# Performance work log

Measured on AMD Instinct MI355X. Metric: run time of the kernel, lower is better.

## Reference

```python
import jax, jax.numpy as jnp
import numpy as np

EPS = 1e-5
LOCAL_WINDOW = 256
NUM_HEADS = 16


def _layernorm(x, g, b):
    m = jnp.mean(x, axis=-1, keepdims=True)
    v = jnp.mean(jnp.square(x - m), axis=-1, keepdims=True)
    return (x - m) * jax.lax.rsqrt(v + EPS) * g + b


def _rotate_half(x):
    x1, x2 = jnp.split(x, 2, axis=-1)
    return jnp.concatenate([-x2, x1], axis=-1)


def _rope_cos_sin(s, d, base=10000.0):
    half = d // 2
    inv_freq = 1.0 / base ** (jnp.arange(half, dtype=jnp.float32) / float(half))
    t = jnp.arange(s, dtype=jnp.float32)
    freqs = jnp.einsum('s,d->sd', t, inv_freq)          # [s, half]
    emb = jnp.concatenate([freqs, freqs], axis=-1)       # [s, d]
    return jnp.cos(emb)[None, None, :, :], jnp.sin(emb)[None, None, :, :]


def setup_inputs() -> dict:
    key = jax.random.key(0)
    ks = jax.random.split(key, 8)
    B, S, D, F = 2, 2048, 1024, 4096
    sc = lambda d: 1.0 / np.sqrt(d)
    return {
        'x': jax.random.normal(ks[0], (B, S, D), jnp.float32),
        'w_qkv': jax.random.normal(ks[1], (D, 3 * D), jnp.float32) * sc(D),
        'w_out': jax.random.normal(ks[2], (D, D), jnp.float32) * sc(D),
        'g1': jnp.ones((D,), jnp.float32),
        'b1': jnp.zeros((D,), jnp.float32),
        'g2': jnp.ones((D,), jnp.float32),
        'b2': jnp.zeros((D,), jnp.float32),
        'w_gate': jax.random.normal(ks[3], (D, F), jnp.float32) * sc(D),
        'b_gate': jnp.zeros((F,), jnp.float32),
        'w_up': jax.random.normal(ks[4], (D, F), jnp.float32) * sc(D),
        'b_up': jnp.zeros((F,), jnp.float32),
        'w_down': jax.random.normal(ks[5], (F, D), jnp.float32) * sc(F),
        'b_down': jnp.zeros((D,), jnp.float32),
    }


def reference(x, w_qkv, w_out, g1, b1, g2, b2, w_gate, b_gate, w_up, b_up, w_down, b_down):
    B, S, D = x.shape
    H = NUM_HEADS
    hd = D // H

    # ---- pre-norm + RoPE self-attention ----
    y = _layernorm(x, g1, b1)
    qkv = jnp.einsum('bsd,de->bse', y, w_qkv)
    q, k, v = jnp.split(qkv, 3, axis=-1)
    split_heads = lambda t: t.reshape(B, S, H, hd).transpose(0, 2, 1, 3)  # [b,h,s,hd]
    q, k, v = split_heads(q), split_heads(k), split_heads(v)

    cos, sin = _rope_cos_sin(S, hd)
    q = q * cos + _rotate_half(q) * sin
    k = k * cos + _rotate_half(k) * sin

    scale = float(hd) ** -0.5
    logits = jnp.einsum('bhid,bhjd->bhij', q, k) * scale

    i = jnp.arange(S)[:, None]
    j = jnp.arange(S)[None, :]
    can = (jnp.abs(j - i) <= LOCAL_WINDOW) & (j <= i)    # local + causal band
    logits = jnp.where(can[None, None], logits, jnp.float32(-1e9))

    attn = jax.nn.softmax(logits, axis=-1)
    o = jnp.einsum('bhij,bhjd->bhid', attn, v)
    o = o.transpose(0, 2, 1, 3).reshape(B, S, D)
    x = x + jnp.einsum('bsd,de->bse', o, w_out)

    # ---- pre-norm + SwiGLU MLP ----
    y = _layernorm(x, g2, b2)
    gate = jnp.einsum('bsd,df->bsf', y, w_gate) + b_gate
    up = jnp.einsum('bsd,df->bsf', y, w_up) + b_up
    gated = gate * jax.nn.silu(up)
    x = x + jnp.einsum('bsf,fd->bsd', gated, w_down) + b_down
    return x
```

## Files before the change

### kernel.cpp

```cpp
#include <hip/hip_runtime.h>

typedef unsigned short u16;
typedef unsigned long long u64;
typedef __attribute__((ext_vector_type(8))) short bf16x8;
typedef __attribute__((ext_vector_type(4))) float f32x4;

__device__ inline u16 f2bf(float f) {
  unsigned int u = __float_as_uint(f);
  u += 0x7fffu + ((u >> 16) & 1u);
  return (u16)(u >> 16);
}
__device__ inline float bf2f(u16 h) { return __uint_as_float(((unsigned int)h) << 16); }

__device__ inline void gload_lds16(const void* gp, void* lp) {
  __builtin_amdgcn_global_load_lds(
      (const __attribute__((address_space(1))) unsigned int*)gp,
      (__attribute__((address_space(3))) unsigned int*)lp, 16, 0, 0);
}

__global__ __launch_bounds__(256) void ln_kernel(const float* __restrict__ x,
                                                 const float* __restrict__ g,
                                                 const float* __restrict__ beta,
                                                 u16* __restrict__ y) {
  __shared__ float red[8];
  const int row = blockIdx.x;
  const int t = threadIdx.x;
  const float4 xv = *(const float4*)(x + (long)row * 1024 + t * 4);
  float s = xv.x + xv.y + xv.z + xv.w;
  float sq = xv.x * xv.x + xv.y * xv.y + xv.z * xv.z + xv.w * xv.w;
#pragma unroll
  for (int d = 1; d < 64; d <<= 1) {
    s += __shfl_xor(s, d);
    sq += __shfl_xor(sq, d);
  }
  if ((t & 63) == 0) { red[t >> 6] = s; red[4 + (t >> 6)] = sq; }
  __syncthreads();
  s = red[0] + red[1] + red[2] + red[3];
  sq = red[4] + red[5] + red[6] + red[7];
  const float mean = s * (1.f / 1024.f);
  const float var = sq * (1.f / 1024.f) - mean * mean;
  const float inv = rsqrtf(var + 1e-5f);
  float xe[4] = {xv.x, xv.y, xv.z, xv.w};
  u16 ov[4];
#pragma unroll
  for (int e = 0; e < 4; ++e)
    ov[e] = f2bf((xe[e] - mean) * inv * g[t * 4 + e] + beta[t * 4 + e]);
  *(u64*)(y + (long)row * 1024 + t * 4) = *(u64*)ov;
}

__global__ __launch_bounds__(256) void transpose_bf16(const float* __restrict__ in,
                                                      u16* __restrict__ out,
                                                      int R, int C) {
  __shared__ float tile[64][33];
  const int t = threadIdx.x;
  const int tx = t & 31, ty = t >> 5;
  const int rx = t & 63, cy = t >> 6;
  const long r0 = (long)blockIdx.y * 64, c0 = (long)blockIdx.x * 32;
#pragma unroll
  for (int i = 0; i < 8; ++i)
    tile[ty + i * 8][tx] = in[(r0 + ty + i * 8) * C + c0 + tx];
  __syncthreads();
#pragma unroll
  for (int i = 0; i < 8; ++i)
    out[(c0 + i * 4 + cy) * R + r0 + rx] = f2bf(tile[rx][i * 4 + cy]);
}

__global__ __launch_bounds__(256) void transpose_v(const u16* __restrict__ vv,
                                                   u16* __restrict__ vt) {
  __shared__ u16 tile[64][72];
  const int bh = blockIdx.y;
  const long s0 = (long)blockIdx.x * 64;
  const int t = threadIdx.x;
  const int r = t >> 3, cc = (t & 7) * 8;
  const long src = ((long)(bh >> 4) * 2048 + s0) * 1024 + (bh & 15) * 64;
  *(bf16x8*)&tile[r][cc] = *(const bf16x8*)(vv + src + (long)r * 1024 + cc);
  *(bf16x8*)&tile[r + 32][cc] = *(const bf16x8*)(vv + src + (long)(r + 32) * 1024 + cc);
  __syncthreads();
  const int d = t >> 3, sx = (t & 7) * 8;
  u16 o0[8], o1[8];
#pragma unroll
  for (int e = 0; e < 8; ++e) { o0[e] = tile[sx + e][d]; o1[e] = tile[sx + e][d + 32]; }
  const long dst = (long)bh * 64 * 2048 + s0;
  *(bf16x8*)(vt + dst + (long)d * 2048 + sx) = *(bf16x8*)o0;
  *(bf16x8*)(vt + dst + (long)(d + 32) * 2048 + sx) = *(bf16x8*)o1;
}

__global__ __launch_bounds__(256) void rope_kernel(const u16* __restrict__ qkv,
                                                   u16* __restrict__ qr,
                                                   u16* __restrict__ kr,
                                                   u16* __restrict__ vv) {
  const int row = blockIdx.x;
  const int s = row & 2047;
  const int t = threadIdx.x;
  const u16* base = qkv + (long)row * 3072;
  const long orow = (long)row * 1024;
#pragma unroll
  for (int rep = 0; rep < 2; ++rep) {
    const int p = rep * 256 + t;
    const int h = p >> 5, d0 = p & 31;
    const float inv = exp2f((float)d0 * (-13.287712379549449f / 32.f));
    const float ang = (float)s * inv;
    float sn, cs;
    sincosf(ang, &sn, &cs);
    const int c1 = h * 64 + d0, c2 = c1 + 32;
    float x1 = bf2f(base[c1]), x2 = bf2f(base[c2]);
    qr[orow + c1] = f2bf((x1 * cs - x2 * sn) * 0.125f);
    qr[orow + c2] = f2bf((x2 * cs + x1 * sn) * 0.125f);
    float y1 = bf2f(base[1024 + c1]), y2 = bf2f(base[1024 + c2]);
    kr[orow + c1] = f2bf(y1 * cs - y2 * sn);
    kr[orow + c2] = f2bf(y2 * cs + y1 * sn);
  }
  *(u64*)(vv + orow + t * 4) = *(const u64*)(base + 2048 + t * 4);
}

__global__ __launch_bounds__(64, 4) void attn_kernel(const u16* __restrict__ qr,
                                                     const u16* __restrict__ kr,
                                                     const u16* __restrict__ vt,
                                                     u16* __restrict__ o) {
  __shared__ __attribute__((aligned(16))) u16 Pl[16][40];
  int wg = blockIdx.x;
  wg = (wg & 7) * 512 + (wg >> 3);
  const int qt = wg & 127;
  const int bh = wg >> 7;
  const int qs = qt * 16;
  const int l = threadIdx.x;
  const int lr = l & 15, lg = l >> 4;
  const long bho = (long)(bh >> 4) * 2048 * 1024 + (long)(bh & 15) * 64;
  const long vtb = (long)bh * 64 * 2048;

  const u16* qp = qr + bho + (long)(qs + lr) * 1024 + lg * 8;
  const bf16x8 aq0 = *(const bf16x8*)qp;
  const bf16x8 aq1 = *(const bf16x8*)(qp + 32);

  f32x4 oacc[4];
#pragma unroll
  for (int nt = 0; nt < 4; ++nt) { oacc[nt][0] = 0.f; oacc[nt][1] = 0.f; oacc[nt][2] = 0.f; oacc[nt][3] = 0.f; }
  float m_[4], ls[4];
#pragma unroll
  for (int r = 0; r < 4; ++r) { m_[r] = -1e30f; ls[r] = 0.f; }

  for (int ch = 0; ch < 9; ++ch) {
    const int j0 = qs - 256 + ch * 32;
    if (j0 + 32 <= 0) continue;

    const int jc0u = j0 + lr;
    const int jc1u = j0 + 16 + lr;
    const int jc0 = min(max(jc0u, 0), 2047);
    const int jc1 = min(max(jc1u, 0), 2047);
    const u16* kp0 = kr + bho + (long)jc0 * 1024 + lg * 8;
    const u16* kp1 = kr + bho + (long)jc1 * 1024 + lg * 8;
    const bf16x8 b00 = *(const bf16x8*)kp0;
    const bf16x8 b01 = *(const bf16x8*)(kp0 + 32);
    const bf16x8 b10 = *(const bf16x8*)kp1;
    const bf16x8 b11 = *(const bf16x8*)(kp1 + 32);

    f32x4 z; z[0] = 0.f; z[1] = 0.f; z[2] = 0.f; z[3] = 0.f;
    f32x4 s0 = __builtin_amdgcn_mfma_f32_16x16x32_bf16(aq0, b00, z, 0, 0, 0);
    s0 = __builtin_amdgcn_mfma_f32_16x16x32_bf16(aq1, b01, s0, 0, 0, 0);
    f32x4 s1 = __builtin_amdgcn_mfma_f32_16x16x32_bf16(aq0, b10, z, 0, 0, 0);
    s1 = __builtin_amdgcn_mfma_f32_16x16x32_bf16(aq1, b11, s1, 0, 0, 0);

    float p0[4], p1[4], al[4];
#pragma unroll
    for (int r = 0; r < 4; ++r) {
      const int qg = qs + lg * 4 + r;
      const bool v0 = (jc0u >= 0) & (jc0u <= qg) & (qg - jc0u <= 256);
      const bool v1 = (jc1u >= 0) & (jc1u <= qg) & (qg - jc1u <= 256);
      const float t0 = v0 ? s0[r] : -1e30f;
      const float t1 = v1 ? s1[r] : -1e30f;
      float mx = fmaxf(t0, t1);
      mx = fmaxf(mx, __shfl_xor(mx, 1));
      mx = fmaxf(mx, __shfl_xor(mx, 2));
      mx = fmaxf(mx, __shfl_xor(mx, 4));
      mx = fmaxf(mx, __shfl_xor(mx, 8));
      const float mn = fmaxf(m_[r], mx);
      if (mn < -1e29f) {
        al[r] = 1.f; p0[r] = 0.f; p1[r] = 0.f;
      } else {
        al[r] = __expf(m_[r] - mn);
        p0[r] = (t0 < -1e29f) ? 0.f : __expf(t0 - mn);
        p1[r] = (t1 < -1e29f) ? 0.f : __expf(t1 - mn);
      }
      m_[r] = mn;
      float rs = p0[r] + p1[r];
      rs += __shfl_xor(rs, 1);
      rs += __shfl_xor(rs, 2);
      rs += __shfl_xor(rs, 4);
      rs += __shfl_xor(rs, 8);
      ls[r] = ls[r] * al[r] + rs;
    }
#pragma unroll
    for (int r = 0; r < 4; ++r) {
      Pl[lg * 4 + r][lr] = f2bf(p0[r]);
      Pl[lg * 4 + r][lr + 16] = f2bf(p1[r]);
    }
    asm volatile("s_waitcnt lgkmcnt(0)" ::: "memory");
    const bf16x8 pa = *(const bf16x8*)(&Pl[lr][lg * 8]);

    const int jb = min(max(j0 + lg * 8, 0), 2040);
    const u16* vp = vt + vtb + (long)lr * 2048 + jb;
#pragma unroll
    for (int nt = 0; nt < 4; ++nt) {
      const bf16x8 bv = *(const bf16x8*)(vp + (long)(nt * 16) * 2048);
      f32x4 oa = oacc[nt];
#pragma unroll
      for (int r = 0; r < 4; ++r) oa[r] *= al[r];
      oacc[nt] = __builtin_amdgcn_mfma_f32_16x16x32_bf16(pa, bv, oa, 0, 0, 0);
    }
  }
#pragma unroll
  for (int nt = 0; nt < 4; ++nt)
#pragma unroll
    for (int r = 0; r < 4; ++r) {
      const long qg = qs + lg * 4 + r;
      o[bho + qg * 1024 + nt * 16 + lr] = f2bf(oacc[nt][r] / ls[r]);
    }
}

__device__ __forceinline__ void stage_half(u16* lds, int ldsbase,
                                           const u16* gp, int ld, int col,
                                           int tid, int w) {
  const int r0 = tid >> 3;
  const int sw = ((tid & 7) ^ (r0 & 7)) << 3;
  gload_lds16(gp + (long)r0 * ld + col + sw, lds + ldsbase + w * 512);
  gload_lds16(gp + (long)(r0 + 64) * ld + col + sw, lds + ldsbase + 4096 + w * 512);
}

template <int EPI>
__global__ __launch_bounds__(512, 2) void gemm8p(const u16* __restrict__ A,
                                                 const u16* __restrict__ BT,
                                                 u16* __restrict__ Cb,
                                                 const float* __restrict__ bias,
                                                 const u16* __restrict__ gate,
                                                 float* __restrict__ Cf0,
                                                 float* __restrict__ Cf1,
                                                 int M, int N, int Kfull, int Kl) {
  __shared__ __attribute__((aligned(16))) u16 lds[65536];
  const int tid = threadIdx.x;
  const int w = tid >> 6, l = tid & 63;
  const int lr = l & 15, lg = l >> 4;
  const int l7 = l & 7;
  const int wr = w >> 2, wc = w & 3;
  const int nbx = N >> 8, nby = M >> 8;
  int wg = blockIdx.x;
  { const int cpx = gridDim.x >> 3; wg = (wg & 7) * cpx + (wg >> 3); }
  const int z = wg / (nbx * nby);
  const int rem = wg % (nbx * nby);
  const long m0 = (long)(rem / nbx) * 256;
  const long n0 = (long)(rem % nbx) * 256;
  const long koff = (long)z * Kl;
  const int NT = Kl >> 6;

  f32x4 acc[8][4];
#pragma unroll
  for (int i = 0; i < 8; ++i)
#pragma unroll
    for (int j = 0; j < 4; ++j) { acc[i][j][0] = 0.f; acc[i][j][1] = 0.f; acc[i][j][2] = 0.f; acc[i][j][3] = 0.f; }

  const u16* Alo = A + m0 * Kfull + koff;
  const u16* Ahi = A + (m0 + 128) * Kfull + koff;
  const u16* Blo = BT + n0 * Kfull + koff;
  const u16* Bhi = BT + (n0 + 128) * Kfull + koff;

  stage_half(lds, 0, Alo, Kfull, 0, tid, w);
  stage_half(lds, 8192, Ahi, Kfull, 0, tid, w);
  stage_half(lds, 32768, Blo, Kfull, 0, tid, w);
  stage_half(lds, 40960, Bhi, Kfull, 0, tid, w);
  stage_half(lds, 49152, Blo, Kfull, 64, tid, w);
  stage_half(lds, 57344, Bhi, Kfull, 64, tid, w);
  asm volatile("s_waitcnt vmcnt(4)" ::: "memory");
  __builtin_amdgcn_s_barrier();

  for (int t = 0; t < NT; ++t) {
    const int p = t & 1;
    const int baA = (p * 2 + wr) * 8192;
    const int bB = 32768 + p * 16384;
    bf16x8 b[4][2];
#pragma unroll
    for (int q = 0; q < 4; ++q) {
      bf16x8 a[2][2];
#pragma unroll
      for (int m2 = 0; m2 < 2; ++m2) {
        const int rowA = (q * 2 + m2) * 16 + lr;
#pragma unroll
        for (int kh = 0; kh < 2; ++kh)
          a[m2][kh] = *(const bf16x8*)(lds + baA + rowA * 64 + (((kh * 4 + lg) ^ l7) << 3));
      }
      if (q == 0) {
#pragma unroll
        for (int fn = 0; fn < 4; ++fn) {
          const int rb = wc * 64 + fn * 16 + lr;
#pragma unroll
          for (int kh = 0; kh < 2; ++kh)
            b[fn][kh] = *(const bf16x8*)(lds + bB + (rb >> 7) * 8192 + (rb & 127) * 64 + (((kh * 4 + lg) ^ l7) << 3));
        }
      }
      if (q == 0 && t + 1 < NT) stage_half(lds, ((p ^ 1) * 2 + 0) * 8192, Alo, Kfull, (t + 1) * 64, tid, w);
      if (q == 1 && t + 1 < NT) stage_half(lds, ((p ^ 1) * 2 + 1) * 8192, Ahi, Kfull, (t + 1) * 64, tid, w);
      if (q == 2 && t + 2 < NT) stage_half(lds, 32768 + (p * 2 + 0) * 8192, Blo, Kfull, (t + 2) * 64, tid, w);
      if (q == 3 && t + 2 < NT) stage_half(lds, 32768 + (p * 2 + 1) * 8192, Bhi, Kfull, (t + 2) * 64, tid, w);

      __builtin_amdgcn_s_barrier();
      asm volatile("s_waitcnt lgkmcnt(0)" ::: "memory");
      __builtin_amdgcn_s_setprio(1);
#pragma unroll
      for (int m2 = 0; m2 < 2; ++m2)
#pragma unroll
        for (int fn = 0; fn < 4; ++fn)
#pragma unroll
          for (int kh = 0; kh < 2; ++kh)
            acc[q * 2 + m2][fn] = __builtin_amdgcn_mfma_f32_16x16x32_bf16(a[m2][kh], b[fn][kh], acc[q * 2 + m2][fn], 0, 0, 0);
      __builtin_amdgcn_s_setprio(0);
      if (q == 3) {
        if (t + 2 < NT) { asm volatile("s_waitcnt vmcnt(4)" ::: "memory"); }
        else            { asm volatile("s_waitcnt vmcnt(0)" ::: "memory"); }
      }
      __builtin_amdgcn_s_barrier();
    }
  }

  float* Cf = nullptr;
  if constexpr (EPI == 0) Cf = (z < 2 ? Cf0 : Cf1) + (long)(z & 1) * M * N;

#pragma unroll
  for (int fm = 0; fm < 8; ++fm) {
    const long mr = m0 + wr * 128 + fm * 16 + lg * 4;
#pragma unroll
    for (int fn = 0; fn < 4; ++fn) {
      const long nc = n0 + wc * 64 + fn * 16 + lr;
#pragma unroll
      for (int r = 0; r < 4; ++r) {
        const long idx = (mr + r) * N + nc;
        const float v = acc[fm][fn][r];
        if constexpr (EPI == 5) {
          Cb[idx] = f2bf(v);
        } else if constexpr (EPI == 2) {
          Cb[idx] = f2bf(v + bias[nc]);
        } else if constexpr (EPI == 3) {
          const float u = v + bias[nc];
          const float sg = 1.f / (1.f + __expf(-u));
          Cb[idx] = f2bf(bf2f(gate[idx]) * u * sg);
        } else {
          Cf[idx] = v;
        }
      }
    }
  }
}

__global__ __launch_bounds__(256) void combine_ln(const float* __restrict__ p0,
                                                  const float* __restrict__ p1,
                                                  const float* __restrict__ x,
                                                  const float* __restrict__ g,
                                                  const float* __restrict__ beta,
                                                  float* __restrict__ x1,
                                                  u16* __restrict__ y) {
  __shared__ float red[8];
  const long MN = (long)4096 * 1024;
  const int row = blockIdx.x;
  const int t = threadIdx.x;
  const long base = (long)row * 1024 + t * 4;
  const float4 a = *(const float4*)(p0 + base);
  const float4 b = *(const float4*)(p0 + MN + base);
  const float4 c = *(const float4*)(p1 + base);
  const float4 d = *(const float4*)(p1 + MN + base);
  const float4 r = *(const float4*)(x + base);
  float v[4] = {a.x + b.x + c.x + d.x + r.x, a.y + b.y + c.y + d.y + r.y,
                a.z + b.z + c.z + d.z + r.z, a.w + b.w + c.w + d.w + r.w};
  *(float4*)(x1 + base) = *(float4*)v;
  float s = v[0] + v[1] + v[2] + v[3];
  float sq = v[0] * v[0] + v[1] * v[1] + v[2] * v[2] + v[3] * v[3];
#pragma unroll
  for (int dd = 1; dd < 64; dd <<= 1) {
    s += __shfl_xor(s, dd);
    sq += __shfl_xor(sq, dd);
  }
  if ((t & 63) == 0) { red[t >> 6] = s; red[4 + (t >> 6)] = sq; }
  __syncthreads();
  s = red[0] + red[1] + red[2] + red[3];
  sq = red[4] + red[5] + red[6] + red[7];
  const float mean = s * (1.f / 1024.f);
  const float var = sq * (1.f / 1024.f) - mean * mean;
  const float inv = rsqrtf(var + 1e-5f);
  u16 ov[4];
#pragma unroll
  for (int e = 0; e < 4; ++e)
    ov[e] = f2bf((v[e] - mean) * inv * g[t * 4 + e] + beta[t * 4 + e]);
  *(u64*)(y + base) = *(u64*)ov;
}

__global__ __launch_bounds__(256) void combine4(const float* __restrict__ p0,
                                                const float* __restrict__ p1,
                                                const float* __restrict__ res,
                                                const float* __restrict__ bias,
                                                float* __restrict__ out) {
  const long MN = (long)4096 * 1024;
  const long i = ((long)blockIdx.x * 256 + threadIdx.x) * 4;
  const float4 a = *(const float4*)(p0 + i);
  const float4 b = *(const float4*)(p0 + MN + i);
  const float4 c = *(const float4*)(p1 + i);
  const float4 d = *(const float4*)(p1 + MN + i);
  const float4 r = *(const float4*)(res + i);
  const float4 bb = *(const float4*)(bias + (int)(i & 1023));
  float4 o;
  o.x = a.x + b.x + c.x + d.x + r.x + bb.x;
  o.y = a.y + b.y + c.y + d.y + r.y + bb.y;
  o.z = a.z + b.z + c.z + d.z + r.z + bb.z;
  o.w = a.w + b.w + c.w + d.w + r.w + bb.w;
  *(float4*)(out + i) = o;
}

extern "C" void kernel_launch(void* const* d_in, const int* in_sizes, int n_in,
                              void* d_out, int out_size, void* d_ws, size_t ws_size,
                              hipStream_t stream) {
  (void)in_sizes; (void)n_in; (void)out_size; (void)ws_size;
  const float* x      = (const float*)d_in[0];
  const float* w_qkv  = (const float*)d_in[1];
  const float* w_out  = (const float*)d_in[2];
  const float* g1     = (const float*)d_in[3];
  const float* b1     = (const float*)d_in[4];
  const float* g2     = (const float*)d_in[5];
  const float* b2     = (const float*)d_in[6];
  const float* w_gate = (const float*)d_in[7];
  const float* b_gate = (const float*)d_in[8];
  const float* w_up   = (const float*)d_in[9];
  const float* b_up   = (const float*)d_in[10];
  const float* w_down = (const float*)d_in[11];
  const float* b_down = (const float*)d_in[12];
  float* out = (float*)d_out;

  const size_t MB = 1u << 20;
  char* ws = (char*)d_ws;
  u16*   wdownT = (u16*)(ws + 0 * MB);
  u16*   y      = (u16*)(ws + 8 * MB);
  u16*   wqkvT  = (u16*)(ws + 16 * MB);
  u16*   woutT  = (u16*)(ws + 22 * MB);
  u16*   wgateT = (u16*)(ws + 24 * MB);
  u16*   wupT   = (u16*)(ws + 32 * MB);
  u16*   qkv    = (u16*)(ws + 40 * MB);
  u16*   vt     = (u16*)(ws + 40 * MB);
  float* x1     = (float*)(ws + 40 * MB);
  u16*   o_     = (u16*)(ws + 56 * MB);
  u16*   qr_    = (u16*)(ws + 64 * MB);
  u16*   kr_    = (u16*)(ws + 72 * MB);
  u16*   vv_    = (u16*)(ws + 80 * MB);
  float* part   = (float*)(ws + 64 * MB);
  u16*   gated  = (u16*)(ws + 64 * MB);
  u16*   gbuf   = (u16*)(ws + 96 * MB);
  float* pd0    = (float*)(ws + 8 * MB);
  float* pd1    = (float*)(ws + 96 * MB);

  const dim3 blk(256);
  transpose_bf16<<<dim3(3072 / 32, 1024 / 64), blk, 0, stream>>>(w_qkv, wqkvT, 1024, 3072);
  transpose_bf16<<<dim3(1024 / 32, 1024 / 64), blk, 0, stream>>>(w_out, woutT, 1024, 1024);
  transpose_bf16<<<dim3(4096 / 32, 1024 / 64), blk, 0, stream>>>(w_gate, wgateT, 1024, 4096);
  transpose_bf16<<<dim3(4096 / 32, 1024 / 64), blk, 0, stream>>>(w_up, wupT, 1024, 4096);
  transpose_bf16<<<dim3(1024 / 32, 4096 / 64), blk, 0, stream>>>(w_down, wdownT, 4096, 1024);

  ln_kernel<<<4096, blk, 0, stream>>>(x, g1, b1, y);
  gemm8p<5><<<dim3((3072 / 256) * (4096 / 256)), dim3(512), 0, stream>>>(
      y, wqkvT, qkv, nullptr, nullptr, nullptr, nullptr, 4096, 3072, 1024, 1024);
  rope_kernel<<<4096, blk, 0, stream>>>(qkv, qr_, kr_, vv_);
  transpose_v<<<dim3(32, 32), blk, 0, stream>>>(vv_, vt);
  attn_kernel<<<4096, dim3(64), 0, stream>>>(qr_, kr_, vt, o_);
  gemm8p<0><<<dim3(4 * 16 * 4), dim3(512), 0, stream>>>(
      o_, woutT, nullptr, nullptr, nullptr, part, part + (long)2 * 4096 * 1024,
      4096, 1024, 1024, 256);
  combine_ln<<<4096, blk, 0, stream>>>(part, part + (long)2 * 4096 * 1024, x, g2, b2, x1, y);
  gemm8p<2><<<dim3((4096 / 256) * (4096 / 256)), dim3(512), 0, stream>>>(
      y, wgateT, gbuf, b_gate, nullptr, nullptr, nullptr, 4096, 4096, 1024, 1024);
  gemm8p<3><<<dim3((4096 / 256) * (4096 / 256)), dim3(512), 0, stream>>>(
      y, wupT, gated, b_up, gbuf, nullptr, nullptr, 4096, 4096, 1024, 1024);
  gemm8p<0><<<dim3(4 * 16 * 4), dim3(512), 0, stream>>>(
      gated, wdownT, nullptr, nullptr, nullptr, pd0, pd1, 4096, 1024, 4096, 1024);
  combine4<<<4096, blk, 0, stream>>>(pd0, pd1, x1, b_down, out);
}
```

Before: 287.3 us.

## Fuse RoPE and V transpose into QKV GEMM epilogue; triple-buffer A tiles

Removes the separate rope and V-transpose kernels by applying rotary embedding and head-major V transpose in a new epilogue of the QKV GEMM. The epilogue reads a precomputed cos/sin table built by a new small kernel. The GEMM mainloop now triple-buffers A tiles, which grows LDS to 160KB per block and prefetches two tiles ahead. This saves a round trip of the qkv intermediate through memory and two launches. The price is higher LDS use, which may lower occupancy, and scattered epilogue stores.

```diff
diff --git a/kernel.cpp b/kernel.cpp
--- a/kernel.cpp
+++ b/kernel.cpp
@@ -65,52 +65,14 @@
     out[(c0 + i * 4 + cy) * R + r0 + rx] = f2bf(tile[rx][i * 4 + cy]);
 }
 
-__global__ __launch_bounds__(256) void transpose_v(const u16* __restrict__ vv,
-                                                   u16* __restrict__ vt) {
-  __shared__ u16 tile[64][72];
-  const int bh = blockIdx.y;
-  const long s0 = (long)blockIdx.x * 64;
-  const int t = threadIdx.x;
-  const int r = t >> 3, cc = (t & 7) * 8;
-  const long src = ((long)(bh >> 4) * 2048 + s0) * 1024 + (bh & 15) * 64;
-  *(bf16x8*)&tile[r][cc] = *(const bf16x8*)(vv + src + (long)r * 1024 + cc);
-  *(bf16x8*)&tile[r + 32][cc] = *(const bf16x8*)(vv + src + (long)(r + 32) * 1024 + cc);
-  __syncthreads();
-  const int d = t >> 3, sx = (t & 7) * 8;
-  u16 o0[8], o1[8];
-#pragma unroll
-  for (int e = 0; e < 8; ++e) { o0[e] = tile[sx + e][d]; o1[e] = tile[sx + e][d + 32]; }
-  const long dst = (long)bh * 64 * 2048 + s0;
-  *(bf16x8*)(vt + dst + (long)d * 2048 + sx) = *(bf16x8*)o0;
-  *(bf16x8*)(vt + dst + (long)(d + 32) * 2048 + sx) = *(bf16x8*)o1;
-}
-
-__global__ __launch_bounds__(256) void rope_kernel(const u16* __restrict__ qkv,
-                                                   u16* __restrict__ qr,
-                                                   u16* __restrict__ kr,
-                                                   u16* __restrict__ vv) {
-  const int row = blockIdx.x;
-  const int s = row & 2047;
-  const int t = threadIdx.x;
-  const u16* base = qkv + (long)row * 3072;
-  const long orow = (long)row * 1024;
-#pragma unroll
-  for (int rep = 0; rep < 2; ++rep) {
-    const int p = rep * 256 + t;
-    const int h = p >> 5, d0 = p & 31;
-    const float inv = exp2f((float)d0 * (-13.287712379549449f / 32.f));
-    const float ang = (float)s * inv;
-    float sn, cs;
-    sincosf(ang, &sn, &cs);
-    const int c1 = h * 64 + d0, c2 = c1 + 32;
-    float x1 = bf2f(base[c1]), x2 = bf2f(base[c2]);
-    qr[orow + c1] = f2bf((x1 * cs - x2 * sn) * 0.125f);
-    qr[orow + c2] = f2bf((x2 * cs + x1 * sn) * 0.125f);
-    float y1 = bf2f(base[1024 + c1]), y2 = bf2f(base[1024 + c2]);
-    kr[orow + c1] = f2bf(y1 * cs - y2 * sn);
-    kr[orow + c2] = f2bf(y2 * cs + y1 * sn);
-  }
-  *(u64*)(vv + orow + t * 4) = *(const u64*)(base + 2048 + t * 4);
+__global__ __launch_bounds__(256) void trig_kernel(float* __restrict__ tbl) {
+  const int i = blockIdx.x * 256 + threadIdx.x;
+  const int s = i >> 5, d0 = i & 31;
+  const float inv = exp2f((float)d0 * (-13.287712379549449f / 32.f));
+  float sn, cs;
+  sincosf((float)s * inv, &sn, &cs);
+  tbl[i] = cs;
+  tbl[65536 + i] = sn;
 }
 
 __global__ __launch_bounds__(64, 4) void attn_kernel(const u16* __restrict__ qr,
@@ -234,8 +196,11 @@
                                                  const u16* __restrict__ gate,
                                                  float* __restrict__ Cf0,
                                                  float* __restrict__ Cf1,
+                                                 u16* __restrict__ P1,
+                                                 u16* __restrict__ P2,
+                                                 const float* __restrict__ tbl,
                                                  int M, int N, int Kfull, int Kl) {
-  __shared__ __attribute__((aligned(16))) u16 lds[65536];
+  __shared__ __attribute__((aligned(16))) u16 lds[81920];
   const int tid = threadIdx.x;
   const int w = tid >> 6, l = tid & 63;
   const int lr = l & 15, lg = l >> 4;
@@ -264,17 +229,21 @@
 
   stage_half(lds, 0, Alo, Kfull, 0, tid, w);
   stage_half(lds, 8192, Ahi, Kfull, 0, tid, w);
-  stage_half(lds, 32768, Blo, Kfull, 0, tid, w);
-  stage_half(lds, 40960, Bhi, Kfull, 0, tid, w);
-  stage_half(lds, 49152, Blo, Kfull, 64, tid, w);
-  stage_half(lds, 57344, Bhi, Kfull, 64, tid, w);
-  asm volatile("s_waitcnt vmcnt(4)" ::: "memory");
+  stage_half(lds, 49152, Blo, Kfull, 0, tid, w);
+  stage_half(lds, 57344, Bhi, Kfull, 0, tid, w);
+  stage_half(lds, 16384, Alo, Kfull, 64, tid, w);
+  stage_half(lds, 24576, Ahi, Kfull, 64, tid, w);
+  stage_half(lds, 65536, Blo, Kfull, 64, tid, w);
+  stage_half(lds, 73728, Bhi, Kfull, 64, tid, w);
+  asm volatile("s_waitcnt vmcnt(8)" ::: "memory");
   __builtin_amdgcn_s_barrier();
 
   for (int t = 0; t < NT; ++t) {
+    const int abuf = t % 3;
+    int sA = abuf + 2; if (sA >= 3) sA -= 3;
     const int p = t & 1;
-    const int baA = (p * 2 + wr) * 8192;
-    const int bB = 32768 + p * 16384;
+    const int baA = abuf * 16384 + wr * 8192;
+    const int bB = 49152 + p * 16384;
     bf16x8 b[4][2];
 #pragma unroll
     for (int q = 0; q < 4; ++q) {
@@ -295,10 +264,12 @@
             b[fn][kh] = *(const bf16x8*)(lds + bB + (rb >> 7) * 8192 + (rb & 127) * 64 + (((kh * 4 + lg) ^ l7) << 3));
         }
       }
-      if (q == 0 && t + 1 < NT) stage_half(lds, ((p ^ 1) * 2 + 0) * 8192, Alo, Kfull, (t + 1) * 64, tid, w);
-      if (q == 1 && t + 1 < NT) stage_half(lds, ((p ^ 1) * 2 + 1) * 8192, Ahi, Kfull, (t + 1) * 64, tid, w);
-      if (q == 2 && t + 2 < NT) stage_half(lds, 32768 + (p * 2 + 0) * 8192, Blo, Kfull, (t + 2) * 64, tid, w);
-      if (q == 3 && t + 2 < NT) stage_half(lds, 32768 + (p * 2 + 1) * 8192, Bhi, Kfull, (t + 2) * 64, tid, w);
+      if (t + 2 < NT) {
+        if (q == 0) stage_half(lds, sA * 16384, Alo, Kfull, (t + 2) * 64, tid, w);
+        if (q == 1) stage_half(lds, sA * 16384 + 8192, Ahi, Kfull, (t + 2) * 64, tid, w);
+        if (q == 2) stage_half(lds, bB, Blo, Kfull, (t + 2) * 64, tid, w);
+        if (q == 3) stage_half(lds, bB + 8192, Bhi, Kfull, (t + 2) * 64, tid, w);
+      }
 
       __builtin_amdgcn_s_barrier();
       asm volatile("s_waitcnt lgkmcnt(0)" ::: "memory");
@@ -312,11 +283,56 @@
             acc[q * 2 + m2][fn] = __builtin_amdgcn_mfma_f32_16x16x32_bf16(a[m2][kh], b[fn][kh], acc[q * 2 + m2][fn], 0, 0, 0);
       __builtin_amdgcn_s_setprio(0);
       if (q == 3) {
-        if (t + 2 < NT) { asm volatile("s_waitcnt vmcnt(4)" ::: "memory"); }
+        if (t + 2 < NT) { asm volatile("s_waitcnt vmcnt(8)" ::: "memory"); }
         else            { asm volatile("s_waitcnt vmcnt(0)" ::: "memory"); }
       }
       __builtin_amdgcn_s_barrier();
     }
+  }
+
+  if constexpr (EPI == 6) {
+    const int regn = (int)((n0 + wc * 64) >> 10);
+    if (regn < 2) {
+      const float scale = (regn == 0) ? 0.125f : 1.f;
+      u16* dst = (regn == 0) ? Cb : P1;
+      const int cbase = (int)(n0 & 1023) + wc * 64 + lr;
+#pragma unroll
+      for (int fm = 0; fm < 8; ++fm) {
+        const long mr = m0 + wr * 128 + fm * 16 + lg * 4;
+#pragma unroll
+        for (int fn = 0; fn < 2; ++fn) {
+          const int c1 = cbase + fn * 16;
+          const int d0 = fn * 16 + lr;
+#pragma unroll
+          for (int r = 0; r < 4; ++r) {
+            const long row = mr + r;
+            const int s = (int)(row & 2047);
+            const float cs = tbl[(s << 5) + d0];
+            const float sn = tbl[65536 + (s << 5) + d0];
+            const float x1v = acc[fm][fn][r], x2v = acc[fm][fn + 2][r];
+            dst[row * 1024 + c1] = f2bf((x1v * cs - x2v * sn) * scale);
+            dst[row * 1024 + c1 + 32] = f2bf((x2v * cs + x1v * sn) * scale);
+          }
+        }
+      }
+    } else {
+#pragma unroll
+      for (int fm = 0; fm < 8; ++fm) {
+        const long mr = m0 + wr * 128 + fm * 16 + lg * 4;
+        const int bb = (int)(mr >> 11);
+        const int s = (int)(mr & 2047);
+#pragma unroll
+        for (int fn = 0; fn < 4; ++fn) {
+          const int ncv = (int)(n0 - 2048) + wc * 64 + fn * 16 + lr;
+          const int h = ncv >> 6, d = ncv & 63;
+          u16 pk[4];
+#pragma unroll
+          for (int r = 0; r < 4; ++r) pk[r] = f2bf(acc[fm][fn][r]);
+          *(u64*)(P2 + (long)(bb * 16 + h) * 131072 + (long)d * 2048 + s) = *(u64*)pk;
+        }
+      }
+    }
+    return;
   }
 
   float* Cf = nullptr;
@@ -340,7 +356,7 @@
           const float u = v + bias[nc];
           const float sg = 1.f / (1.f + __expf(-u));
           Cb[idx] = f2bf(bf2f(gate[idx]) * u * sg);
-        } else {
+        } else if constexpr (EPI == 0) {
           Cf[idx] = v;
         }
       }
@@ -437,18 +453,18 @@
   u16*   woutT  = (u16*)(ws + 22 * MB);
   u16*   wgateT = (u16*)(ws + 24 * MB);
   u16*   wupT   = (u16*)(ws + 32 * MB);
-  u16*   qkv    = (u16*)(ws + 40 * MB);
-  u16*   vt     = (u16*)(ws + 40 * MB);
-  float* x1     = (float*)(ws + 40 * MB);
-  u16*   o_     = (u16*)(ws + 56 * MB);
-  u16*   qr_    = (u16*)(ws + 64 * MB);
-  u16*   kr_    = (u16*)(ws + 72 * MB);
-  u16*   vv_    = (u16*)(ws + 80 * MB);
-  float* part   = (float*)(ws + 64 * MB);
-  u16*   gated  = (u16*)(ws + 64 * MB);
-  u16*   gbuf   = (u16*)(ws + 96 * MB);
-  float* pd0    = (float*)(ws + 8 * MB);
-  float* pd1    = (float*)(ws + 96 * MB);
+  u16*   qr_    = (u16*)(ws + 40 * MB);
+  u16*   kr_    = (u16*)(ws + 48 * MB);
+  u16*   vt     = (u16*)(ws + 56 * MB);
+  float* trig   = (float*)(ws + 64 * MB);
+  u16*   o_     = (u16*)(ws + 64 * MB);
+  float* part0  = (float*)(ws + 72 * MB);
+  float* part1  = (float*)(ws + 104 * MB);
+  float* x1     = (float*)(ws + 56 * MB);
+  u16*   gbuf   = (u16*)(ws + 72 * MB);
+  u16*   gated  = (u16*)(ws + 104 * MB);
+  float* pd0    = (float*)(ws + 16 * MB);
+  float* pd1    = (float*)(ws + 72 * MB);
 
   const dim3 blk(256);
   transpose_bf16<<<dim3(3072 / 32, 1024 / 64), blk, 0, stream>>>(w_qkv, wqkvT, 1024, 3072);
@@ -456,22 +472,25 @@
   transpose_bf16<<<dim3(4096 / 32, 1024 / 64), blk, 0, stream>>>(w_gate, wgateT, 1024, 4096);
   transpose_bf16<<<dim3(4096 / 32, 1024 / 64), blk, 0, stream>>>(w_up, wupT, 1024, 4096);
   transpose_bf16<<<dim3(1024 / 32, 4096 / 64), blk, 0, stream>>>(w_down, wdownT, 4096, 1024);
+  trig_kernel<<<256, blk, 0, stream>>>(trig);
 
   ln_kernel<<<4096, blk, 0, stream>>>(x, g1, b1, y);
-  gemm8p<5><<<dim3((3072 / 256) * (4096 / 256)), dim3(512), 0, stream>>>(
-      y, wqkvT, qkv, nullptr, nullptr, nullptr, nullptr, 4096, 3072, 1024, 1024);
-  rope_kernel<<<4096, blk, 0, stream>>>(qkv, qr_, kr_, vv_);
-  transpose_v<<<dim3(32, 32), blk, 0, stream>>>(vv_, vt);
+  gemm8p<6><<<dim3((3072 / 256) * (4096 / 256)), dim3(512), 0, stream>>>(
+      y, wqkvT, qr_, nullptr, nullptr, nullptr, nullptr, kr_, vt, trig,
+      4096, 3072, 1024, 1024);
   attn_kernel<<<4096, dim3(64), 0, stream>>>(qr_, kr_, vt, o_);
   gemm8p<0><<<dim3(4 * 16 * 4), dim3(512), 0, stream>>>(
-      o_, woutT, nullptr, nullptr, nullptr, part, part + (long)2 * 4096 * 1024,
+      o_, woutT, nullptr, nullptr, nullptr, part0, part1, nullptr, nullptr, nullptr,
       4096, 1024, 1024, 256);
-  combine_ln<<<4096, blk, 0, stream>>>(part, part + (long)2 * 4096 * 1024, x, g2, b2, x1, y);
+  combine_ln<<<4096, blk, 0, stream>>>(part0, part1, x, g2, b2, x1, y);
   gemm8p<2><<<dim3((4096 / 256) * (4096 / 256)), dim3(512), 0, stream>>>(
-      y, wgateT, gbuf, b_gate, nullptr, nullptr, nullptr, 4096, 4096, 1024, 1024);
+      y, wgateT, gbuf, b_gate, nullptr, nullptr, nullptr, nullptr, nullptr, nullptr,
+      4096, 4096, 1024, 1024);
   gemm8p<3><<<dim3((4096 / 256) * (4096 / 256)), dim3(512), 0, stream>>>(
-      y, wupT, gated, b_up, gbuf, nullptr, nullptr, 4096, 4096, 1024, 1024);
+      y, wupT, gated, b_up, gbuf, nullptr, nullptr, nullptr, nullptr, nullptr,
+      4096, 4096, 1024, 1024);
   gemm8p<0><<<dim3(4 * 16 * 4), dim3(512), 0, stream>>>(
-      gated, wdownT, nullptr, nullptr, nullptr, pd0, pd1, 4096, 1024, 4096, 1024);
+      gated, wdownT, nullptr, nullptr, nullptr, pd0, pd1, nullptr, nullptr, nullptr,
+      4096, 1024, 4096, 1024);
   combine4<<<4096, blk, 0, stream>>>(pd0, pd1, x1, b_down, out);
 }
```

New measurement: 283.8 us. About the same (-1.2%).
